# Optimization experiments

Hardware: AMD Instinct MI355X
Metric: run time of the kernel (lower is better)

## Reference

```python
import jax, jax.numpy as jnp
import numpy as np

N_WAY = 5
NKPTS = 17
EMBED = 512
N_SUPPORT = 25  # 5-way 5-shot
N_QUERY = 65536


def setup_inputs() -> dict:
    key = jax.random.key(0)
    ks = jax.random.split(key, 12)
    def lin(k, fan_in, fan_out):
        return jax.random.normal(k, (fan_in, fan_out), jnp.float32) / np.float32(np.sqrt(fan_in))
    return {
        'support_features': jax.random.normal(ks[0], (1, N_SUPPORT, EMBED), jnp.float32),
        'support_keypoints': jax.random.uniform(ks[1], (N_SUPPORT, NKPTS, 2), jnp.float32),
        'query_features': jax.random.normal(ks[2], (N_QUERY, EMBED), jnp.float32),
        'image_coords': jax.random.uniform(ks[3], (N_QUERY, 2), jnp.float32) * 512.0,
        'W1': lin(ks[4], EMBED, EMBED), 'b1': jnp.zeros((EMBED,), jnp.float32),
        'W2': lin(ks[5], EMBED, EMBED), 'b2': jnp.zeros((EMBED,), jnp.float32),
        'Wo1': lin(ks[6], EMBED, EMBED // 2), 'bo1': jnp.zeros((EMBED // 2,), jnp.float32),
        'Wo2': lin(ks[7], EMBED // 2, 2), 'bo2': jnp.zeros((2,), jnp.float32),
        'Wc1': lin(ks[8], EMBED, EMBED // 2), 'bc1': jnp.zeros((EMBED // 2,), jnp.float32),
        'Wc2': lin(ks[9], EMBED // 2, 1), 'bc2': jnp.zeros((1,), jnp.float32),
        'temperature': jnp.float32(1.0),
    }


def reference(support_features, support_keypoints, query_features, image_coords,
              W1, b1, W2, b2, Wo1, bo1, Wo2, bo2, Wc1, bc1, Wc2, bc2, temperature):
    eps = 1e-8
    nkpts = support_keypoints.shape[1]
    n_query = query_features.shape[0]
    D = query_features.shape[-1]

    # --- compute_prototypes (batch_size == 1; per-kpt prototype identical by construction) ---
    sf = support_features.reshape(-1, D)                      # [Ns, D]
    h = jnp.maximum(sf @ W1 + b1, 0.0) @ W2 + b2              # prototype_net MLP
    n_per = h.shape[0] // N_WAY
    proto_way = h.reshape(N_WAY, n_per, D).mean(axis=1)       # [n_way, D]
    prototypes = jnp.broadcast_to(proto_way[:, None, :], (N_WAY, nkpts, D))

    # --- compute_distances: 1 - cosine_sim, scaled by temperature ---
    qn = jnp.linalg.norm(query_features, axis=-1)             # [Nq]
    pn = jnp.linalg.norm(proto_way, axis=-1)                  # [n_way]
    sim = (query_features @ proto_way.T) / jnp.maximum(qn[:, None] * pn[None, :], eps)
    dist_way = (1.0 - sim) / temperature                      # [Nq, n_way]
    distances = jnp.broadcast_to(dist_way[:, :, None], (n_query, N_WAY, nkpts))

    # --- predict_keypoints ---
    # avg over kpts is a no-op (identical per kpt); argmin over ways
    class_predictions = jnp.argmin(dist_way, axis=1)          # [Nq] int
    # softmax over a single scalar == 1.0, so keypoints == offset broadcast over kpts
    offset = jnp.maximum(query_features @ Wo1 + bo1, 0.0) @ Wo2 + bo2   # [Nq, 2]
    conf = jax.nn.sigmoid(jnp.maximum(query_features @ Wc1 + bc1, 0.0) @ Wc2 + bc2)  # [Nq, 1]
    keypoints = jnp.broadcast_to(offset[:, None, :], (n_query, nkpts, 2))
    keypoints = jax.nn.sigmoid(keypoints) * image_coords[:, None, :]    # image_coords provided
    confidence = jnp.broadcast_to(conf, (n_query, nkpts))

    return keypoints, confidence, distances, class_predictions, prototypes
```

## Files before the change

### kernel.cpp

```cpp
#include <hip/hip_runtime.h>
#include <hip/hip_bf16.h>

#define NQ 65536
#define DIM 512
#define HID 256
#define NWAY 5
#define NKPTS 17

typedef short bf16x8 __attribute__((ext_vector_type(8)));
typedef float f32x4 __attribute__((ext_vector_type(4)));
typedef _Float16 half8 __attribute__((ext_vector_type(8)));

static __device__ __forceinline__ unsigned short f2bf(float f) {
    unsigned int x = __float_as_uint(f);
    unsigned int r = (x + 0x7fffu + ((x >> 16) & 1u)) >> 16;
    return (unsigned short)r;
}
static __device__ __forceinline__ int swz(int r) { return (r ^ (r >> 2)) & 3; }

static __device__ __forceinline__ void ldg_lds16(const void* g, void* l) {
    __builtin_amdgcn_global_load_lds(
        (const __attribute__((address_space(1))) unsigned int*)g,
        (__attribute__((address_space(3))) unsigned int*)l, 16, 0, 0);
}

__global__ __launch_bounds__(256) void k_l1(const float* __restrict__ sf,
                                            const float* __restrict__ W1, const float* __restrict__ b1,
                                            const float* __restrict__ Wo1, const float* __restrict__ Wc1,
                                            float* __restrict__ ws_h1, unsigned short* __restrict__ wbT) {
    int bx = blockIdx.x, t = threadIdx.x;
    if (bx < 50) {
        __shared__ float s_sf[DIM];
        int s = bx >> 1, c = (bx & 1) * 256 + t;
        s_sf[t] = sf[s * DIM + t];
        s_sf[t + 256] = sf[s * DIM + 256 + t];
        __syncthreads();
        float acc = 0.0f;
        #pragma unroll 8
        for (int k = 0; k < DIM; k++) acc += W1[k * DIM + c] * s_sf[k];
        ws_h1[s * DIM + c] = fmaxf(acc + b1[c], 0.0f);
    } else {
        __shared__ unsigned short T[64][72];
        int tb = bx - 50;
        const float* src = (tb < 32) ? Wo1 : Wc1;
        int cofs = (tb < 32) ? 0 : 256;
        int tt = tb & 31;
        int kt = tt >> 2;
        int ct = tt & 3;
        int i = t >> 2;
        int qd = t & 3;
        const float* rp = src + (size_t)(kt * 64 + i) * HID + ct * 64 + qd * 16;
        #pragma unroll
        for (int v = 0; v < 4; v++) {
            float4 x = *(const float4*)(rp + v * 4);
            T[qd * 16 + v * 4 + 0][i] = f2bf(x.x);
            T[qd * 16 + v * 4 + 1][i] = f2bf(x.y);
            T[qd * 16 + v * 4 + 2][i] = f2bf(x.z);
            T[qd * 16 + v * 4 + 3][i] = f2bf(x.w);
        }
        __syncthreads();
        int j = t >> 2;
        int part = t & 3;
        uint4 o0 = *(const uint4*)&T[j][part * 16];
        uint4 o1 = *(const uint4*)&T[j][part * 16 + 8];
        int col = cofs + ct * 64 + j;
        int k0 = kt * 64 + part * 16;
        int it0 = k0 >> 5;
        int kc0 = (k0 >> 3) & 3;
        int s = swz(j & 15);
        unsigned short* base = wbT + it0 * 16384 + col * 32;
        *(uint4*)(base + ((kc0 ^ s) * 8)) = o0;
        *(uint4*)(base + (((kc0 + 1) ^ s) * 8)) = o1;
    }
}

__global__ __launch_bounds__(256) void k_l2(const float* __restrict__ ws_h1,
                                            const float* __restrict__ W2, const float* __restrict__ b2,
                                            float* __restrict__ ws_proto, float* __restrict__ ws_pn) {
    __shared__ float s_m[DIM];
    __shared__ float red[256];
    int w = blockIdx.x, t = threadIdx.x;
    for (int k = t; k < DIM; k += 256) {
        float m = 0.0f;
        #pragma unroll
        for (int s = 0; s < 5; s++) m += ws_h1[(w * 5 + s) * DIM + k];
        s_m[k] = m * 0.2f;
    }
    __syncthreads();
    float a0 = 0.0f, a1 = 0.0f;
    int c0 = t, c1 = t + 256;
    #pragma unroll 8
    for (int k = 0; k < DIM; k++) {
        float mk = s_m[k];
        a0 += W2[k * DIM + c0] * mk;
        a1 += W2[k * DIM + c1] * mk;
    }
    float v0 = a0 + b2[c0], v1 = a1 + b2[c1];
    ws_proto[w * DIM + c0] = v0;
    ws_proto[w * DIM + c1] = v1;
    red[t] = v0 * v0 + v1 * v1;
    __syncthreads();
    for (int s2 = 128; s2 > 0; s2 >>= 1) {
        if (t < s2) red[t] += red[t + s2];
        __syncthreads();
    }
    if (t == 0) ws_pn[w] = sqrtf(red[0]);
}

__global__ __launch_bounds__(256) void k_cd(const float* __restrict__ qf,
                                            const float* __restrict__ ws_proto, const float* __restrict__ ws_pn,
                                            const float* __restrict__ temp_p,
                                            float* __restrict__ out_dist, float* __restrict__ out_class,
                                            float* __restrict__ out_proto,
                                            unsigned short* __restrict__ qb, int do_qb) {
    __shared__ float dl[32][5];
    __shared__ float cl[32];
    int bx = blockIdx.x, t = threadIdx.x;
    int wv = t >> 6, lane = t & 63;

    if (bx < NWAY * NKPTS && t < 128) {
        f32x4 v = *(const f32x4*)(ws_proto + (bx / NKPTS) * DIM + t * 4);
        *(f32x4*)(out_proto + (size_t)bx * DIM + t * 4) = v;
    }

    float p[NWAY][8];
    #pragma unroll
    for (int w = 0; w < NWAY; w++) {
        f32x4 u0 = *(const f32x4*)(ws_proto + w * DIM + lane * 8);
        f32x4 u1 = *(const f32x4*)(ws_proto + w * DIM + lane * 8 + 4);
        p[w][0] = u0[0]; p[w][1] = u0[1]; p[w][2] = u0[2]; p[w][3] = u0[3];
        p[w][4] = u1[0]; p[w][5] = u1[1]; p[w][6] = u1[2]; p[w][7] = u1[3];
    }
    float pn[NWAY];
    #pragma unroll
    for (int w = 0; w < NWAY; w++) pn[w] = ws_pn[w];
    float invt = 1.0f / temp_p[0];

    int itc = lane >> 2, kcc = lane & 3;
    #pragma unroll
    for (int i = 0; i < 8; i++) {
        int rloc = wv * 8 + i;
        size_t rq = (size_t)bx * 32 + rloc;
        const float4* qp = (const float4*)(qf + rq * DIM + lane * 8);
        float4 a = qp[0], b = qp[1];
        float qv[8] = {a.x, a.y, a.z, a.w, b.x, b.y, b.z, b.w};
        if (do_qb) {
            unsigned int p0 = f2bf(qv[0]) | ((unsigned int)f2bf(qv[1]) << 16);
            unsigned int p1 = f2bf(qv[2]) | ((unsigned int)f2bf(qv[3]) << 16);
            unsigned int p2 = f2bf(qv[4]) | ((unsigned int)f2bf(qv[5]) << 16);
            unsigned int p3 = f2bf(qv[6]) | ((unsigned int)f2bf(qv[7]) << 16);
            int row = (int)(rq & 63);
            size_t mb2 = rq >> 6;
            char* dst = (char*)qb + mb2 * 65536 + itc * 4096 + row * 64 + ((kcc ^ swz(row)) << 4);
            *(uint4*)dst = make_uint4(p0, p1, p2, p3);
        }
        float s[6] = {0, 0, 0, 0, 0, 0};
        #pragma unroll
        for (int j = 0; j < 8; j++) {
            float v = qv[j];
            s[5] += v * v;
            #pragma unroll
            for (int w = 0; w < NWAY; w++) s[w] += v * p[w][j];
        }
        #pragma unroll
        for (int off = 32; off > 0; off >>= 1)
            #pragma unroll
            for (int k = 0; k < 6; k++) s[k] += __shfl_xor(s[k], off, 64);
        if (lane == 0) {
            float qn = sqrtf(s[5]);
            float mv = 1e30f;
            int ami = 0;
            #pragma unroll
            for (int w = 0; w < NWAY; w++) {
                float den = fmaxf(qn * pn[w], 1e-8f);
                float d = (1.0f - s[w] / den) * invt;
                dl[rloc][w] = d;
                if (d < mv) { mv = d; ami = w; }
            }
            cl[rloc] = (float)ami;
        }
    }
    __syncthreads();
    for (int i = t; i < 32 * NWAY * NKPTS; i += 256) {
        int q = i / (NWAY * NKPTS);
        int rem = i - q * (NWAY * NKPTS);
        out_dist[(size_t)bx * 32 * (NWAY * NKPTS) + i] = dl[q][rem / NKPTS];
    }
    if (t < 32) out_class[(size_t)bx * 32 + t] = cl[t];
}

static __device__ __forceinline__ void epilogue(f32x4 acc[4][4], char* smem, int mb, int nb,
                                                int t, int wv, int lane, int r,
                                                const float* __restrict__ bo1, const float* __restrict__ Wo2,
                                                const float* __restrict__ bo2,
                                                const float* __restrict__ bc1, const float* __restrict__ Wc2,
                                                const float* __restrict__ bc2,
                                                const float* __restrict__ ic,
                                                float* __restrict__ out_kp, float* __restrict__ out_conf) {
    _Float16* hlds = (_Float16*)smem;
    float* offlds = (float*)(smem + 33792);
    const float* bias = nb ? bc1 : bo1;
    #pragma unroll
    for (int nt = 0; nt < 4; nt++) {
        int cl = wv * 64 + nt * 16 + r;
        float bv = bias[cl];
        #pragma unroll
        for (int mt = 0; mt < 4; mt++)
            #pragma unroll
            for (int rg = 0; rg < 4; rg++) {
                int ml = mt * 16 + (lane >> 4) * 4 + rg;
                float v = acc[mt][nt][rg] + bv;
                hlds[ml * 264 + cl] = (_Float16)fmaxf(v, 0.0f);
            }
    }
    __syncthreads();
    if (nb == 0) {
        if (t < 64) {
            float ox = bo2[0], oy = bo2[1];
            for (int c0 = 0; c0 < 256; c0 += 8) {
                half8 hv = *(const half8*)(hlds + t * 264 + c0);
                #pragma unroll
                for (int j = 0; j < 8; j++) {
                    float hf = (float)hv[j];
                    ox += hf * Wo2[(c0 + j) * 2];
                    oy += hf * Wo2[(c0 + j) * 2 + 1];
                }
            }
            offlds[t * 2] = ox;
            offlds[t * 2 + 1] = oy;
        }
        __syncthreads();
        for (int i = t; i < 64 * 34; i += 256) {
            int q = i / 34;
            int rem = i - q * 34;
            int j = rem & 1;
            size_t Q = (size_t)mb * 64 + q;
            float o = offlds[q * 2 + j];
            float sg = 1.0f / (1.0f + __expf(-o));
            out_kp[Q * 34 + rem] = sg * ic[Q * 2 + j];
        }
    } else {
        if (t < 64) {
            float cl2 = bc2[0];
            for (int c0 = 0; c0 < 256; c0 += 8) {
                half8 hv = *(const half8*)(hlds + t * 264 + c0);
                #pragma unroll
                for (int j = 0; j < 8; j++) cl2 += (float)hv[j] * Wc2[c0 + j];
            }
            offlds[t] = 1.0f / (1.0f + __expf(-cl2));
        }
        __syncthreads();
        for (int i = t; i < 64 * 17; i += 256) {
            int q = i / 17;
            out_conf[(size_t)mb * 64 * 17 + i] = offlds[q];
        }
    }
}

__global__ __launch_bounds__(256) void k_ga(const unsigned short* __restrict__ qb,
                                            const unsigned short* __restrict__ wbT,
                                            const float* __restrict__ bo1, const float* __restrict__ Wo2,
                                            const float* __restrict__ bo2,
                                            const float* __restrict__ bc1, const float* __restrict__ Wc2,
                                            const float* __restrict__ bc2,
                                            const float* __restrict__ ic,
                                            float* __restrict__ out_kp, float* __restrict__ out_conf) {
    __shared__ __align__(16) char smem[40960];
    int mb = blockIdx.x >> 1;
    int nb = blockIdx.x & 1;
    int t = threadIdx.x;
    int wv = t >> 6;
    int lane = t & 63;
    int r = lane & 15;
    int qg = lane >> 4;
    int as = (qg ^ swz(r)) << 4;

    f32x4 acc[4][4];
    #pragma unroll
    for (int i = 0; i < 4; i++)
        #pragma unroll
        for (int j = 0; j < 4; j++) { f32x4 z = {0.f, 0.f, 0.f, 0.f}; acc[i][j] = z; }

    const char* aG = (const char*)qb + (size_t)mb * 65536 + wv * 1024 + lane * 16;
    const char* bG = (const char*)wbT + nb * 16384 + wv * 4096 + lane * 16;

    #pragma unroll
    for (int b = 0; b < 2; b++) {
        ldg_lds16(aG + b * 4096, smem + b * 4096 + wv * 1024);
        #pragma unroll
        for (int i = 0; i < 4; i++)
            ldg_lds16(bG + b * 32768 + i * 1024, smem + 8192 + b * 16384 + wv * 4096 + i * 1024);
    }
    __builtin_amdgcn_sched_barrier(0);

    for (int p = 0; p < 16; p++) {
        if (p < 15) __builtin_amdgcn_s_waitcnt(0x0F75);
        else        __builtin_amdgcn_s_waitcnt(0x0F70);
        __builtin_amdgcn_s_barrier();
        __builtin_amdgcn_sched_barrier(0);
        int bi = p & 1;
        const char* ab = smem + bi * 4096;
        const char* bb = smem + 8192 + bi * 16384;
        bf16x8 af[4], bf[4];
        #pragma unroll
        for (int mt = 0; mt < 4; mt++)
            af[mt] = *(const bf16x8*)(ab + (mt * 16 + r) * 64 + as);
        #pragma unroll
        for (int nt = 0; nt < 4; nt++)
            bf[nt] = *(const bf16x8*)(bb + (wv * 64 + nt * 16 + r) * 64 + as);
        #pragma unroll
        for (int mt = 0; mt < 4; mt++)
            #pragma unroll
            for (int nt = 0; nt < 4; nt++)
                acc[mt][nt] = __builtin_amdgcn_mfma_f32_16x16x32_bf16(af[mt], bf[nt], acc[mt][nt], 0, 0, 0);
        __builtin_amdgcn_sched_barrier(0);
        __builtin_amdgcn_s_barrier();
        if (p < 14) {
            int b2 = p + 2;
            ldg_lds16(aG + b2 * 4096, smem + bi * 4096 + wv * 1024);
            #pragma unroll
            for (int i = 0; i < 4; i++)
                ldg_lds16(bG + (size_t)b2 * 32768 + i * 1024, smem + 8192 + bi * 16384 + wv * 4096 + i * 1024);
        }
        __builtin_amdgcn_sched_barrier(0);
    }
    __syncthreads();
    epilogue(acc, smem, mb, nb, t, wv, lane, r, bo1, Wo2, bo2, bc1, Wc2, bc2, ic, out_kp, out_conf);
}

__global__ __launch_bounds__(256) void k_gs(const float* __restrict__ qf,
                                            const unsigned short* __restrict__ wbT,
                                            const float* __restrict__ bo1, const float* __restrict__ Wo2,
                                            const float* __restrict__ bo2,
                                            const float* __restrict__ bc1, const float* __restrict__ Wc2,
                                            const float* __restrict__ bc2,
                                            const float* __restrict__ ic,
                                            float* __restrict__ out_kp, float* __restrict__ out_conf) {
    __shared__ __align__(16) char smem[40960];
    int mb = blockIdx.x >> 1;
    int nb = blockIdx.x & 1;
    int t = threadIdx.x;
    int wv = t >> 6;
    int lane = t & 63;
    int r = lane & 15;
    int qg = lane >> 4;
    int as = (qg ^ swz(r)) << 4;

    f32x4 acc[4][4];
    #pragma unroll
    for (int i = 0; i < 4; i++)
        #pragma unroll
        for (int j = 0; j < 4; j++) { f32x4 z = {0.f, 0.f, 0.f, 0.f}; acc[i][j] = z; }

    int am = t >> 2;
    int akc = t & 3;
    const float* aptr = qf + ((size_t)(mb * 64 + am)) * DIM + akc * 8;
    const char* bGb = (const char*)wbT + nb * 16384 + t * 16;
    int awoff = am * 64 + ((akc ^ swz(am)) << 4);

    float4 A0 = *(const float4*)(aptr);
    float4 A1 = *(const float4*)(aptr + 4);
    uint4 Bp[4];
    #pragma unroll
    for (int j = 0; j < 4; j++) Bp[j] = *(const uint4*)(bGb + j * 4096);

    for (int it = 0; it < 16; it++) {
        unsigned int p0 = f2bf(A0.x) | ((unsigned int)f2bf(A0.y) << 16);
        unsigned int p1 = f2bf(A0.z) | ((unsigned int)f2bf(A0.w) << 16);
        unsigned int p2 = f2bf(A1.x) | ((unsigned int)f2bf(A1.y) << 16);
        unsigned int p3 = f2bf(A1.z) | ((unsigned int)f2bf(A1.w) << 16);
        __syncthreads();
        *(uint4*)(smem + awoff) = make_uint4(p0, p1, p2, p3);
        #pragma unroll
        for (int j = 0; j < 4; j++) *(uint4*)(smem + 8192 + j * 4096 + t * 16) = Bp[j];
        __syncthreads();
        if (it < 15) {
            int k1 = (it + 1) * 32;
            A0 = *(const float4*)(aptr + k1);
            A1 = *(const float4*)(aptr + k1 + 4);
            #pragma unroll
            for (int j = 0; j < 4; j++) Bp[j] = *(const uint4*)(bGb + (size_t)(it + 1) * 32768 + j * 4096);
        }
        bf16x8 af[4], bf[4];
        #pragma unroll
        for (int mt = 0; mt < 4; mt++)
            af[mt] = *(const bf16x8*)(smem + (mt * 16 + r) * 64 + as);
        #pragma unroll
        for (int nt = 0; nt < 4; nt++)
            bf[nt] = *(const bf16x8*)(smem + 8192 + (wv * 64 + nt * 16 + r) * 64 + as);
        #pragma unroll
        for (int mt = 0; mt < 4; mt++)
            #pragma unroll
            for (int nt = 0; nt < 4; nt++)
                acc[mt][nt] = __builtin_amdgcn_mfma_f32_16x16x32_bf16(af[mt], bf[nt], acc[mt][nt], 0, 0, 0);
    }
    __syncthreads();
    epilogue(acc, smem, mb, nb, t, wv, lane, r, bo1, Wo2, bo2, bc1, Wc2, bc2, ic, out_kp, out_conf);
}

extern "C" void kernel_launch(void* const* d_in, const int* in_sizes, int n_in,
                              void* d_out, int out_size, void* d_ws, size_t ws_size,
                              hipStream_t stream) {
    const float* sf = (const float*)d_in[0];
    const float* qf = (const float*)d_in[2];
    const float* ic = (const float*)d_in[3];
    const float* W1 = (const float*)d_in[4];
    const float* b1 = (const float*)d_in[5];
    const float* W2 = (const float*)d_in[6];
    const float* b2 = (const float*)d_in[7];
    const float* Wo1 = (const float*)d_in[8];
    const float* bo1 = (const float*)d_in[9];
    const float* Wo2 = (const float*)d_in[10];
    const float* bo2 = (const float*)d_in[11];
    const float* Wc1 = (const float*)d_in[12];
    const float* bc1 = (const float*)d_in[13];
    const float* Wc2 = (const float*)d_in[14];
    const float* bc2 = (const float*)d_in[15];
    const float* temp = (const float*)d_in[16];

    float* out = (float*)d_out;
    float* out_kp = out;
    float* out_conf = out + 2228224;
    float* out_dist = out + 3342336;
    float* out_class = out + 8912896;
    float* out_proto = out + 8978432;

    char* ws = (char*)d_ws;
    float* ws_h1 = (float*)ws;
    float* ws_proto = (float*)(ws + 51200);
    float* ws_pn = (float*)(ws + 61440);
    unsigned short* ws_wbT = (unsigned short*)(ws + 65536);
    unsigned short* ws_qb = (unsigned short*)(ws + 1048576);
    int use_qb = (ws_size >= (size_t)1048576 + 67108864) ? 1 : 0;

    hipLaunchKernelGGL(k_l1, dim3(114), dim3(256), 0, stream, sf, W1, b1, Wo1, Wc1, ws_h1, ws_wbT);
    hipLaunchKernelGGL(k_l2, dim3(5), dim3(256), 0, stream, ws_h1, W2, b2, ws_proto, ws_pn);
    hipLaunchKernelGGL(k_cd, dim3(2048), dim3(256), 0, stream, qf, ws_proto, ws_pn, temp,
                       out_dist, out_class, out_proto, ws_qb, use_qb);
    if (use_qb) {
        hipLaunchKernelGGL(k_ga, dim3(2048), dim3(256), 0, stream, ws_qb, ws_wbT,
                           bo1, Wo2, bo2, bc1, Wc2, bc2, ic, out_kp, out_conf);
    } else {
        hipLaunchKernelGGL(k_gs, dim3(2048), dim3(256), 0, stream, qf, ws_wbT,
                           bo1, Wo2, bo2, bc1, Wc2, bc2, ic, out_kp, out_conf);
    }
}
```

Before: 391.7 us.

## Pre-pack operands in MFMA fragment order and load directly to registers

The bf16 copies of the query and the weights are now written in the exact per-lane MFMA fragment order, so the GEMM kernel reads each fragment straight from global memory into registers. This removes the LDS staging, the async global-to-LDS copies and the per-step barriers. Loads are double-buffered in registers across two k-steps. The cost is that each wave loads its operands independently with no sharing through LDS, which adds global/L2 traffic, and latency hiding now rests on register prefetch instead of the LDS pipeline.

```diff
diff --git a/kernel.cpp b/kernel.cpp
--- a/kernel.cpp
+++ b/kernel.cpp
@@ -16,13 +16,7 @@
     unsigned int r = (x + 0x7fffu + ((x >> 16) & 1u)) >> 16;
     return (unsigned short)r;
 }
-static __device__ __forceinline__ int swz(int r) { return (r ^ (r >> 2)) & 3; }
-
-static __device__ __forceinline__ void ldg_lds16(const void* g, void* l) {
-    __builtin_amdgcn_global_load_lds(
-        (const __attribute__((address_space(1))) unsigned int*)g,
-        (__attribute__((address_space(3))) unsigned int*)l, 16, 0, 0);
-}
+
 
 __global__ __launch_bounds__(256) void k_l1(const float* __restrict__ sf,
                                             const float* __restrict__ W1, const float* __restrict__ b1,
@@ -66,11 +60,11 @@
         int col = cofs + ct * 64 + j;
         int k0 = kt * 64 + part * 16;
         int it0 = k0 >> 5;
-        int kc0 = (k0 >> 3) & 3;
-        int s = swz(j & 15);
-        unsigned short* base = wbT + it0 * 16384 + col * 32;
-        *(uint4*)(base + ((kc0 ^ s) * 8)) = o0;
-        *(uint4*)(base + (((kc0 + 1) ^ s) * 8)) = o1;
+        int qg0 = (k0 & 31) >> 3;
+        int c64 = col >> 6, nt = (col >> 4) & 3, rr = col & 15;
+        char* base = (char*)wbT + (size_t)(it0 * 8 + c64) * 4096 + nt * 1024 + rr * 16;
+        *(uint4*)(base + qg0 * 256) = o0;
+        *(uint4*)(base + (qg0 + 1) * 256) = o1;
     }
 }
 
@@ -136,7 +130,7 @@
     for (int w = 0; w < NWAY; w++) pn[w] = ws_pn[w];
     float invt = 1.0f / temp_p[0];
 
-    int itc = lane >> 2, kcc = lane & 3;
+    int itc = lane >> 2, qgc = lane & 3;
     #pragma unroll
     for (int i = 0; i < 8; i++) {
         int rloc = wv * 8 + i;
@@ -151,7 +145,8 @@
             unsigned int p3 = f2bf(qv[6]) | ((unsigned int)f2bf(qv[7]) << 16);
             int row = (int)(rq & 63);
             size_t mb2 = rq >> 6;
-            char* dst = (char*)qb + mb2 * 65536 + itc * 4096 + row * 64 + ((kcc ^ swz(row)) << 4);
+            int mt = row >> 4, rr = row & 15;
+            char* dst = (char*)qb + mb2 * 65536 + (size_t)(itc * 4 + mt) * 1024 + (qgc * 16 + rr) * 16;
             *(uint4*)dst = make_uint4(p0, p1, p2, p3);
         }
         float s[6] = {0, 0, 0, 0, 0, 0};
@@ -257,7 +252,7 @@
     }
 }
 
-__global__ __launch_bounds__(256) void k_ga(const unsigned short* __restrict__ qb,
+__global__ __launch_bounds__(256) void k_gr(const unsigned short* __restrict__ qb,
                                             const unsigned short* __restrict__ wbT,
                                             const float* __restrict__ bo1, const float* __restrict__ Wo2,
                                             const float* __restrict__ bo2,
@@ -265,15 +260,13 @@
                                             const float* __restrict__ bc2,
                                             const float* __restrict__ ic,
                                             float* __restrict__ out_kp, float* __restrict__ out_conf) {
-    __shared__ __align__(16) char smem[40960];
+    __shared__ __align__(16) char smem[34816];
     int mb = blockIdx.x >> 1;
     int nb = blockIdx.x & 1;
     int t = threadIdx.x;
     int wv = t >> 6;
     int lane = t & 63;
     int r = lane & 15;
-    int qg = lane >> 4;
-    int as = (qg ^ swz(r)) << 4;
 
     f32x4 acc[4][4];
     #pragma unroll
@@ -281,48 +274,36 @@
         #pragma unroll
         for (int j = 0; j < 4; j++) { f32x4 z = {0.f, 0.f, 0.f, 0.f}; acc[i][j] = z; }
 
-    const char* aG = (const char*)qb + (size_t)mb * 65536 + wv * 1024 + lane * 16;
-    const char* bG = (const char*)wbT + nb * 16384 + wv * 4096 + lane * 16;
-
-    #pragma unroll
-    for (int b = 0; b < 2; b++) {
-        ldg_lds16(aG + b * 4096, smem + b * 4096 + wv * 1024);
-        #pragma unroll
-        for (int i = 0; i < 4; i++)
-            ldg_lds16(bG + b * 32768 + i * 1024, smem + 8192 + b * 16384 + wv * 4096 + i * 1024);
-    }
-    __builtin_amdgcn_sched_barrier(0);
-
-    for (int p = 0; p < 16; p++) {
-        if (p < 15) __builtin_amdgcn_s_waitcnt(0x0F75);
-        else        __builtin_amdgcn_s_waitcnt(0x0F70);
-        __builtin_amdgcn_s_barrier();
-        __builtin_amdgcn_sched_barrier(0);
-        int bi = p & 1;
-        const char* ab = smem + bi * 4096;
-        const char* bb = smem + 8192 + bi * 16384;
-        bf16x8 af[4], bf[4];
+    const char* aP = (const char*)qb + (size_t)mb * 65536 + lane * 16;
+    const char* bP = (const char*)wbT + (size_t)(nb * 4 + wv) * 4096 + lane * 16;
+
+    bf16x8 a0[4], b0[4], a1[4], b1[4];
+    #pragma unroll
+    for (int mt = 0; mt < 4; mt++) a0[mt] = *(const bf16x8*)(aP + mt * 1024);
+    #pragma unroll
+    for (int nt = 0; nt < 4; nt++) b0[nt] = *(const bf16x8*)(bP + nt * 1024);
+
+    for (int it = 0; it < 16; it += 2) {
+        #pragma unroll
+        for (int mt = 0; mt < 4; mt++) a1[mt] = *(const bf16x8*)(aP + (size_t)((it + 1) * 4 + mt) * 1024);
+        #pragma unroll
+        for (int nt = 0; nt < 4; nt++) b1[nt] = *(const bf16x8*)(bP + (size_t)(it + 1) * 32768 + nt * 1024);
         #pragma unroll
         for (int mt = 0; mt < 4; mt++)
-            af[mt] = *(const bf16x8*)(ab + (mt * 16 + r) * 64 + as);
-        #pragma unroll
-        for (int nt = 0; nt < 4; nt++)
-            bf[nt] = *(const bf16x8*)(bb + (wv * 64 + nt * 16 + r) * 64 + as);
+            #pragma unroll
+            for (int nt = 0; nt < 4; nt++)
+                acc[mt][nt] = __builtin_amdgcn_mfma_f32_16x16x32_bf16(a0[mt], b0[nt], acc[mt][nt], 0, 0, 0);
+        if (it + 2 < 16) {
+            #pragma unroll
+            for (int mt = 0; mt < 4; mt++) a0[mt] = *(const bf16x8*)(aP + (size_t)((it + 2) * 4 + mt) * 1024);
+            #pragma unroll
+            for (int nt = 0; nt < 4; nt++) b0[nt] = *(const bf16x8*)(bP + (size_t)(it + 2) * 32768 + nt * 1024);
+        }
         #pragma unroll
         for (int mt = 0; mt < 4; mt++)
             #pragma unroll
             for (int nt = 0; nt < 4; nt++)
-                acc[mt][nt] = __builtin_amdgcn_mfma_f32_16x16x32_bf16(af[mt], bf[nt], acc[mt][nt], 0, 0, 0);
-        __builtin_amdgcn_sched_barrier(0);
-        __builtin_amdgcn_s_barrier();
-        if (p < 14) {
-            int b2 = p + 2;
-            ldg_lds16(aG + b2 * 4096, smem + bi * 4096 + wv * 1024);
-            #pragma unroll
-            for (int i = 0; i < 4; i++)
-                ldg_lds16(bG + (size_t)b2 * 32768 + i * 1024, smem + 8192 + bi * 16384 + wv * 4096 + i * 1024);
-        }
-        __builtin_amdgcn_sched_barrier(0);
+                acc[mt][nt] = __builtin_amdgcn_mfma_f32_16x16x32_bf16(a1[mt], b1[nt], acc[mt][nt], 0, 0, 0);
     }
     __syncthreads();
     epilogue(acc, smem, mb, nb, t, wv, lane, r, bo1, Wo2, bo2, bc1, Wc2, bc2, ic, out_kp, out_conf);
@@ -336,7 +317,7 @@
                                             const float* __restrict__ bc2,
                                             const float* __restrict__ ic,
                                             float* __restrict__ out_kp, float* __restrict__ out_conf) {
-    __shared__ __align__(16) char smem[40960];
+    __shared__ __align__(16) char smem[34816];
     int mb = blockIdx.x >> 1;
     int nb = blockIdx.x & 1;
     int t = threadIdx.x;
@@ -344,7 +325,6 @@
     int lane = t & 63;
     int r = lane & 15;
     int qg = lane >> 4;
-    int as = (qg ^ swz(r)) << 4;
 
     f32x4 acc[4][4];
     #pragma unroll
@@ -352,42 +332,25 @@
         #pragma unroll
         for (int j = 0; j < 4; j++) { f32x4 z = {0.f, 0.f, 0.f, 0.f}; acc[i][j] = z; }
 
-    int am = t >> 2;
-    int akc = t & 3;
-    const float* aptr = qf + ((size_t)(mb * 64 + am)) * DIM + akc * 8;
-    const char* bGb = (const char*)wbT + nb * 16384 + t * 16;
-    int awoff = am * 64 + ((akc ^ swz(am)) << 4);
-
-    float4 A0 = *(const float4*)(aptr);
-    float4 A1 = *(const float4*)(aptr + 4);
-    uint4 Bp[4];
-    #pragma unroll
-    for (int j = 0; j < 4; j++) Bp[j] = *(const uint4*)(bGb + j * 4096);
+    const char* bP = (const char*)wbT + (size_t)(nb * 4 + wv) * 4096 + lane * 16;
 
     for (int it = 0; it < 16; it++) {
-        unsigned int p0 = f2bf(A0.x) | ((unsigned int)f2bf(A0.y) << 16);
-        unsigned int p1 = f2bf(A0.z) | ((unsigned int)f2bf(A0.w) << 16);
-        unsigned int p2 = f2bf(A1.x) | ((unsigned int)f2bf(A1.y) << 16);
-        unsigned int p3 = f2bf(A1.z) | ((unsigned int)f2bf(A1.w) << 16);
-        __syncthreads();
-        *(uint4*)(smem + awoff) = make_uint4(p0, p1, p2, p3);
-        #pragma unroll
-        for (int j = 0; j < 4; j++) *(uint4*)(smem + 8192 + j * 4096 + t * 16) = Bp[j];
-        __syncthreads();
-        if (it < 15) {
-            int k1 = (it + 1) * 32;
-            A0 = *(const float4*)(aptr + k1);
-            A1 = *(const float4*)(aptr + k1 + 4);
-            #pragma unroll
-            for (int j = 0; j < 4; j++) Bp[j] = *(const uint4*)(bGb + (size_t)(it + 1) * 32768 + j * 4096);
-        }
         bf16x8 af[4], bf[4];
         #pragma unroll
-        for (int mt = 0; mt < 4; mt++)
-            af[mt] = *(const bf16x8*)(smem + (mt * 16 + r) * 64 + as);
+        for (int mt = 0; mt < 4; mt++) {
+            const float* ap = qf + (size_t)(mb * 64 + mt * 16 + r) * DIM + it * 32 + qg * 8;
+            float4 x0 = *(const float4*)ap;
+            float4 x1 = *(const float4*)(ap + 4);
+            bf16x8 v;
+            v[0] = (short)f2bf(x0.x); v[1] = (short)f2bf(x0.y);
+            v[2] = (short)f2bf(x0.z); v[3] = (short)f2bf(x0.w);
+            v[4] = (short)f2bf(x1.x); v[5] = (short)f2bf(x1.y);
+            v[6] = (short)f2bf(x1.z); v[7] = (short)f2bf(x1.w);
+            af[mt] = v;
+        }
         #pragma unroll
         for (int nt = 0; nt < 4; nt++)
-            bf[nt] = *(const bf16x8*)(smem + 8192 + (wv * 64 + nt * 16 + r) * 64 + as);
+            bf[nt] = *(const bf16x8*)(bP + (size_t)it * 32768 + nt * 1024);
         #pragma unroll
         for (int mt = 0; mt < 4; mt++)
             #pragma unroll
@@ -438,7 +401,7 @@
     hipLaunchKernelGGL(k_cd, dim3(2048), dim3(256), 0, stream, qf, ws_proto, ws_pn, temp,
                        out_dist, out_class, out_proto, ws_qb, use_qb);
     if (use_qb) {
-        hipLaunchKernelGGL(k_ga, dim3(2048), dim3(256), 0, stream, ws_qb, ws_wbT,
+        hipLaunchKernelGGL(k_gr, dim3(2048), dim3(256), 0, stream, ws_qb, ws_wbT,
                            bo1, Wo2, bo2, bc1, Wc2, bc2, ic, out_kp, out_conf);
     } else {
         hipLaunchKernelGGL(k_gs, dim3(2048), dim3(256), 0, stream, qf, ws_wbT,
```

After: 441.2 us. 1.13x slower.
